# Performance work log

Measured on AMD Instinct MI355X. Metric: run time of the kernel, lower is better.

## Reference

```python
import jax, jax.numpy as jnp
import numpy as np

N = 50000      # nodes
E = 800000     # edges (avg degree 16)
D = 96         # input_size == output_size
C = 10         # n_class
STEPS = 4      # num_layers -> GGNN propagation steps


def setup_inputs() -> dict:
    key = jax.random.key(0)
    ks = jax.random.split(key, 12)
    s = 1.0 / np.sqrt(D)
    return {
        "x": jax.random.normal(ks[0], (N, D), dtype=jnp.float32),
        "src": jax.random.randint(ks[1], (E,), 0, N, dtype=jnp.int32),
        "dst": jax.random.randint(ks[2], (E,), 0, N, dtype=jnp.int32),
        # edge message transform (DGL GatedGraphConv: Linear(out, out) per etype, 1 etype)
        "W_e": jax.random.normal(ks[3], (D, D), dtype=jnp.float32) * s,
        "b_e": jax.random.normal(ks[4], (D,), dtype=jnp.float32) * s,
        # GRUCell params (torch layout: rows ordered r, z, n)
        "W_ih": jax.random.normal(ks[5], (3 * D, D), dtype=jnp.float32) * s,
        "W_hh": jax.random.normal(ks[6], (3 * D, D), dtype=jnp.float32) * s,
        "b_ih": jax.random.normal(ks[7], (3 * D,), dtype=jnp.float32) * s,
        "b_hh": jax.random.normal(ks[8], (3 * D,), dtype=jnp.float32) * s,
        # classifier head
        "W_fc": jax.random.normal(ks[9], (C, D), dtype=jnp.float32) * s,
        "b_fc": jax.random.normal(ks[10], (C,), dtype=jnp.float32) * s,
    }


def _gru_cell(a, h, W_ih, W_hh, b_ih, b_hh):
    # torch.nn.GRUCell math; gate order r, z, n
    gx = a @ W_ih.T + b_ih            # [N, 3D]
    gh = h @ W_hh.T + b_hh            # [N, 3D]
    xr, xz, xn = jnp.split(gx, 3, axis=-1)
    hr, hz, hn = jnp.split(gh, 3, axis=-1)
    r = jax.nn.sigmoid(xr + hr)
    z = jax.nn.sigmoid(xz + hz)
    n = jnp.tanh(xn + r * hn)
    return (1.0 - z) * n + z * h


def reference(x, src, dst, W_e, b_e, W_ih, W_hh, b_ih, b_hh, W_fc, b_fc):
    h = x  # in_feats == out_feats, no padding needed
    for _ in range(STEPS):
        m = h @ W_e.T + b_e                                  # per-node transform [N, D]
        a = jax.ops.segment_sum(m[src], dst, num_segments=N) # gather + scatter-add [N, D]
        h = _gru_cell(a, h, W_ih, W_hh, b_ih, b_hh)
    logits = jax.nn.elu(h) @ W_fc.T + b_fc                   # [N, C]
    return logits
```

## Files before the change

kernel.cpp:

```cpp
#include <hip/hip_runtime.h>

static constexpr int D = 96;
static constexpr int G3 = 3 * D;
static constexpr int NSTEPS = 4;
static constexpr int NT = 18;
static constexpr int SCAN_BLK = 1024;
static constexpr int SLP = 104;

typedef __attribute__((ext_vector_type(8))) _Float16 f16x8;
typedef __attribute__((ext_vector_type(4))) _Float16 f16x4;
typedef __attribute__((ext_vector_type(4))) float f32x4;

__device__ __forceinline__ f16x8 load_a_frag(const _Float16* __restrict__ base,
                                             int r0, int lane, int kc) {
  int row = r0 + (lane & 15);
  int k0 = kc * 32 + ((lane >> 4) << 3);
  return *(const f16x8*)(base + (size_t)row * D + k0);
}

__device__ __forceinline__ f16x8 load_b_swz(const _Float16* __restrict__ W,
                                            int t, int kc, int lane) {
  return *(const f16x8*)(W + (((size_t)t * 3 + kc) * 64 + lane) * 8);
}


__global__ void convert_x_kernel(const float* __restrict__ x,
                                 _Float16* __restrict__ h, int total4) {
  int i = blockIdx.x * blockDim.x + threadIdx.x;
  if (i >= total4) return;
  float4 v = ((const float4*)x)[i];
  f16x4 o;
  o[0] = (_Float16)v.x; o[1] = (_Float16)v.y;
  o[2] = (_Float16)v.z; o[3] = (_Float16)v.w;
  *(f16x4*)(h + (size_t)i * 4) = o;
}

__global__ void compute_wx_kernel(const float* __restrict__ Wih,
                                  const float* __restrict__ We,
                                  const float* __restrict__ be,
                                  float* __restrict__ Wx,
                                  float* __restrict__ bxe) {
  int idx = blockIdx.x * blockDim.x + threadIdx.x;
  if (idx < G3 * D) {
    int r = idx / D, k = idx - r * D;
    float acc = 0.f;
    for (int c = 0; c < D; ++c) acc += Wih[r * D + c] * We[c * D + k];
    Wx[idx] = acc;
  } else if (idx < G3 * D + G3) {
    int r = idx - G3 * D;
    float acc = 0.f;
    for (int c = 0; c < D; ++c) acc += Wih[r * D + c] * be[c];
    bxe[r] = acc;
  }
}

__global__ void swizzle_f16_kernel(const float* __restrict__ Wx,
                                   const float* __restrict__ Whh,
                                   _Float16* __restrict__ WxF,
                                   _Float16* __restrict__ WhhF) {
  int idx = blockIdx.x * blockDim.x + threadIdx.x;
  if (idx >= 2 * NT * 3 * 64) return;
  int mat = idx / (NT * 3 * 64);
  int rem = idx - mat * (NT * 3 * 64);
  int t = rem / (3 * 64);
  int rem2 = rem - t * (3 * 64);
  int kc = rem2 >> 6;
  int lane = rem2 & 63;
  int c = t * 16 + (lane & 15);
  int k0 = kc * 32 + ((lane >> 4) << 3);
  const float* W = mat ? Whh : Wx;
  _Float16* dF = mat ? WhhF : WxF;
  f16x8 o;
#pragma unroll
  for (int j = 0; j < 8; ++j) o[j] = (_Float16)W[(size_t)c * D + k0 + j];
  *(f16x8*)(dF + (((size_t)t * 3 + kc) * 64 + lane) * 8) = o;
}


__global__ void hist_kernel(const int* __restrict__ dst, int* __restrict__ counts, int E) {
  int e = blockIdx.x * blockDim.x + threadIdx.x;
  if (e < E) atomicAdd(&counts[dst[e]], 1);
}

__global__ void partial_sum_kernel(const int* __restrict__ counts,
                                   int* __restrict__ blk_sums, int n) {
  __shared__ int red[256];
  int base = blockIdx.x * SCAN_BLK;
  int tid = threadIdx.x;
  int s = 0;
#pragma unroll
  for (int j = 0; j < 4; ++j) {
    int i = base + j * 256 + tid;
    if (i < n) s += counts[i];
  }
  red[tid] = s;
  __syncthreads();
  for (int off = 128; off > 0; off >>= 1) {
    if (tid < off) red[tid] += red[tid + off];
    __syncthreads();
  }
  if (tid == 0) blk_sums[blockIdx.x] = red[0];
}

__global__ void scan_offsets_kernel(const int* __restrict__ blk_sums,
                                    int* __restrict__ blk_off,
                                    int* __restrict__ row_ptr, int nb, int n) {
  __shared__ int lds[64];
  int tid = threadIdx.x;
  if (tid < nb) lds[tid] = blk_sums[tid];
  __syncthreads();
  if (tid == 0) {
    int run = 0;
    for (int i = 0; i < nb; ++i) { blk_off[i] = run; run += lds[i]; }
    row_ptr[n] = run;
  }
}

__global__ void block_scan_kernel(const int* __restrict__ counts,
                                  const int* __restrict__ blk_off,
                                  int* __restrict__ row_ptr, int n) {
  __shared__ int red[256];
  int base = blockIdx.x * SCAN_BLK;
  int tid = threadIdx.x;
  int i0 = base + tid * 4;
  int v0 = 0, v1 = 0, v2 = 0, v3 = 0;
  if (i0 + 3 < n) {
    int4 c = *(const int4*)(counts + i0);
    v0 = c.x; v1 = c.y; v2 = c.z; v3 = c.w;
  } else {
    if (i0 < n) v0 = counts[i0];
    if (i0 + 1 < n) v1 = counts[i0 + 1];
    if (i0 + 2 < n) v2 = counts[i0 + 2];
  }
  int tsum = v0 + v1 + v2 + v3;
  red[tid] = tsum;
  __syncthreads();
  for (int off = 1; off < 256; off <<= 1) {
    int t = (tid >= off) ? red[tid - off] : 0;
    __syncthreads();
    red[tid] += t;
    __syncthreads();
  }
  int excl = blk_off[blockIdx.x] + red[tid] - tsum;
  if (i0 < n) row_ptr[i0] = excl;
  if (i0 + 1 < n) row_ptr[i0 + 1] = excl + v0;
  if (i0 + 2 < n) row_ptr[i0 + 2] = excl + v0 + v1;
  if (i0 + 3 < n) row_ptr[i0 + 3] = excl + v0 + v1 + v2;
}

__global__ void fill_kernel(const int* __restrict__ src, const int* __restrict__ dst,
                            const int* __restrict__ row_ptr,
                            int* __restrict__ fillc, int* __restrict__ csr_src, int E) {
  int e = blockIdx.x * blockDim.x + threadIdx.x;
  if (e >= E) return;
  int t = dst[e];
  int pos = row_ptr[t] + atomicAdd(&fillc[t], 1);
  csr_src[pos] = src[e];
}


__device__ __forceinline__ void store_planes(float* lds, const f32x4* accM,
                                             const f32x4* accE, int main_plane,
                                             int extra_plane, int extra_ct0, int lane) {
  int col_l = lane & 15;
  int rq = (lane >> 4) << 2;
#pragma unroll
  for (int ct = 0; ct < 6; ++ct)
#pragma unroll
    for (int q = 0; q < 4; ++q)
      lds[main_plane * (16 * D) + (rq + q) * D + ct * 16 + col_l] = accM[ct][q];
#pragma unroll
  for (int ct = 0; ct < 3; ++ct)
#pragma unroll
    for (int q = 0; q < 4; ++q)
      lds[extra_plane * (16 * D) + (rq + q) * D + (extra_ct0 + ct) * 16 + col_l] = accE[ct][q];
}

__device__ __forceinline__ void gru_epilogue(const float* lds,
                                             const _Float16* __restrict__ h,
                                             _Float16* __restrict__ hout,
                                             const int* __restrict__ row_ptr,
                                             const float* __restrict__ bxe,
                                             const float* __restrict__ bih,
                                             const float* __restrict__ bhh,
                                             int base_row, int tid) {
#pragma unroll
  for (int j = 0; j < 6; ++j) {
    int e = tid + j * 256;
    int row = e / D;
    int col = e - row * D;
    int grow = base_row + row;
    float degf = (float)(row_ptr[grow + 1] - row_ptr[grow]);
    float R  = lds[e] + lds[16 * D + e];
    float Z  = lds[2 * 16 * D + e] + lds[3 * 16 * D + e];
    float XN = lds[4 * 16 * D + e];
    float HN = lds[5 * 16 * D + e];
    float rg = 1.0f / (1.0f + __expf(-(R + bih[col] + bhh[col] + degf * bxe[col])));
    float zg = 1.0f / (1.0f + __expf(-(Z + bih[D + col] + bhh[D + col] + degf * bxe[D + col])));
    float ng = tanhf(XN + bih[2 * D + col] + degf * bxe[2 * D + col] + rg * (HN + bhh[2 * D + col]));
    float hv = (float)h[(size_t)grow * D + col];
    hout[(size_t)grow * D + col] = (_Float16)((1.0f - zg) * ng + zg * hv);
  }
}

__global__ __launch_bounds__(256) void gru_fused_kernel(
    const _Float16* __restrict__ h, _Float16* __restrict__ hout,
    const int* __restrict__ row_ptr, const int* __restrict__ csr_src,
    const _Float16* __restrict__ WxF, const _Float16* __restrict__ WhhF,
    const float* __restrict__ bxe, const float* __restrict__ bih,
    const float* __restrict__ bhh, int n) {
  __shared__ float lds[6 * 16 * D];
  __shared__ _Float16 sl[32][SLP];
  int r0 = blockIdx.x << 5;
  int w = threadIdx.x >> 6;
  int lane = threadIdx.x & 63;

  {
    int row = threadIdx.x >> 3;
    int part = threadIdx.x & 7;
    int grow = r0 + row;
    float acc[12];
#pragma unroll
    for (int j = 0; j < 12; ++j) acc[j] = 0.f;
    if (grow < n) {
      int beg = row_ptr[grow], end = row_ptr[grow + 1];
      int e = beg;
      for (; e + 1 < end; e += 2) {
        const _Float16* p0 = h + (size_t)csr_src[e] * D + part * 12;
        const _Float16* p1 = h + (size_t)csr_src[e + 1] * D + part * 12;
        f16x4 u0 = *(const f16x4*)(p0), u1 = *(const f16x4*)(p0 + 4), u2 = *(const f16x4*)(p0 + 8);
        f16x4 v0 = *(const f16x4*)(p1), v1 = *(const f16x4*)(p1 + 4), v2 = *(const f16x4*)(p1 + 8);
#pragma unroll
        for (int j = 0; j < 4; ++j) {
          acc[j]     += (float)u0[j] + (float)v0[j];
          acc[4 + j] += (float)u1[j] + (float)v1[j];
          acc[8 + j] += (float)u2[j] + (float)v2[j];
        }
      }
      if (e < end) {
        const _Float16* p0 = h + (size_t)csr_src[e] * D + part * 12;
        f16x4 u0 = *(const f16x4*)(p0), u1 = *(const f16x4*)(p0 + 4), u2 = *(const f16x4*)(p0 + 8);
#pragma unroll
        for (int j = 0; j < 4; ++j) {
          acc[j] += (float)u0[j]; acc[4 + j] += (float)u1[j]; acc[8 + j] += (float)u2[j];
        }
      }
    }
    f16x4 o0, o1, o2;
#pragma unroll
    for (int j = 0; j < 4; ++j) {
      o0[j] = (_Float16)acc[j]; o1[j] = (_Float16)acc[4 + j]; o2[j] = (_Float16)acc[8 + j];
    }
    *(f16x4*)&sl[row][part * 12]     = o0;
    *(f16x4*)&sl[row][part * 12 + 4] = o1;
    *(f16x4*)&sl[row][part * 12 + 8] = o2;
  }
  __syncthreads();

  const int opS = (w < 2) ? 1 : 0;
  const _Float16* WF = opS ? WxF : WhhF;
  const int half = w & 1;
  const int main_t0 = half * 6;
  const int main_plane = half * 2 + (opS ? 0 : 1);
  const int extra_t0 = 12 + half * 3;
  const int extra_ct0 = half * 3;
  const int extra_plane = opS ? 4 : 5;

  f16x8 a0[3], a1[3];
  if (opS) {
#pragma unroll
    for (int kc = 0; kc < 3; ++kc) {
      int k0 = kc * 32 + ((lane >> 4) << 3);
      a0[kc] = *(const f16x8*)&sl[lane & 15][k0];
      a1[kc] = *(const f16x8*)&sl[16 + (lane & 15)][k0];
    }
  } else {
#pragma unroll
    for (int kc = 0; kc < 3; ++kc) {
      a0[kc] = load_a_frag(h, r0, lane, kc);
      a1[kc] = load_a_frag(h, r0 + 16, lane, kc);
    }
  }

  f32x4 accM0[6], accM1[6], accE0[3], accE1[3];
#pragma unroll
  for (int t = 0; t < 6; ++t) {
    accM0[t] = (f32x4){0.f, 0.f, 0.f, 0.f};
    accM1[t] = (f32x4){0.f, 0.f, 0.f, 0.f};
  }
#pragma unroll
  for (int t = 0; t < 3; ++t) {
    accE0[t] = (f32x4){0.f, 0.f, 0.f, 0.f};
    accE1[t] = (f32x4){0.f, 0.f, 0.f, 0.f};
  }

#pragma unroll
  for (int ct = 0; ct < 6; ++ct)
#pragma unroll
    for (int kc = 0; kc < 3; ++kc) {
      f16x8 b = load_b_swz(WF, main_t0 + ct, kc, lane);
      accM0[ct] = __builtin_amdgcn_mfma_f32_16x16x32_f16(a0[kc], b, accM0[ct], 0, 0, 0);
      accM1[ct] = __builtin_amdgcn_mfma_f32_16x16x32_f16(a1[kc], b, accM1[ct], 0, 0, 0);
    }
#pragma unroll
  for (int ct = 0; ct < 3; ++ct)
#pragma unroll
    for (int kc = 0; kc < 3; ++kc) {
      f16x8 b = load_b_swz(WF, extra_t0 + ct, kc, lane);
      accE0[ct] = __builtin_amdgcn_mfma_f32_16x16x32_f16(a0[kc], b, accE0[ct], 0, 0, 0);
      accE1[ct] = __builtin_amdgcn_mfma_f32_16x16x32_f16(a1[kc], b, accE1[ct], 0, 0, 0);
    }

  __syncthreads();
  store_planes(lds, accM0, accE0, main_plane, extra_plane, extra_ct0, lane);
  __syncthreads();
  gru_epilogue(lds, h, hout, row_ptr, bxe, bih, bhh, r0, threadIdx.x);
  __syncthreads();
  if (r0 + 16 < n) {
    store_planes(lds, accM1, accE1, main_plane, extra_plane, extra_ct0, lane);
    __syncthreads();
    gru_epilogue(lds, h, hout, row_ptr, bxe, bih, bhh, r0 + 16, threadIdx.x);
  }
}

__global__ void head_kernel(const _Float16* __restrict__ h,
                            const float* __restrict__ Wfc,
                            const float* __restrict__ bfc,
                            float* __restrict__ out,
                            int n, int C) {
  int idx = blockIdx.x * blockDim.x + threadIdx.x;
  if (idx >= n * C) return;
  int i = idx / C;
  int c = idx - i * C;
  const _Float16* hr = h + (size_t)i * D;
  const float* wr = Wfc + (size_t)c * D;
  float acc = bfc[c];
#pragma unroll 8
  for (int k = 0; k < D; ++k) {
    float hv = (float)hr[k];
    float e = hv > 0.0f ? hv : (__expf(hv) - 1.0f);
    acc += e * wr[k];
  }
  out[idx] = acc;
}

extern "C" void kernel_launch(void* const* d_in, const int* in_sizes, int n_in,
                              void* d_out, int out_size, void* d_ws, size_t ws_size,
                              hipStream_t stream) {
  const float* x    = (const float*)d_in[0];
  const int*   src  = (const int*)d_in[1];
  const int*   dst  = (const int*)d_in[2];
  const float* W_e  = (const float*)d_in[3];
  const float* b_e  = (const float*)d_in[4];
  const float* W_ih = (const float*)d_in[5];
  const float* W_hh = (const float*)d_in[6];
  const float* b_ih = (const float*)d_in[7];
  const float* b_hh = (const float*)d_in[8];
  const float* W_fc = (const float*)d_in[9];
  const float* b_fc = (const float*)d_in[10];

  const int n = in_sizes[0] / D;
  const int E = in_sizes[1];
  const int C = out_size / n;

  _Float16* hA = (_Float16*)d_ws;
  _Float16* hB = hA + (size_t)n * D;
  float* Wx    = (float*)(hB + (size_t)n * D);
  _Float16* WxF  = (_Float16*)(Wx + (size_t)G3 * D);
  _Float16* WhhF = WxF + (size_t)G3 * D;
  float* bxe   = (float*)(WhhF + (size_t)G3 * D);
  int* counts  = (int*)(bxe + G3);
  int* fillc   = counts + n;
  int* row_ptr = fillc + n;
  int* csr_src = row_ptr + (n + 1);
  int* blk_sums = csr_src + E;
  int* blk_off  = blk_sums + 64;

  const int threads = 256;
  const int nb = (n + SCAN_BLK - 1) / SCAN_BLK;

  (void)hipMemsetAsync(counts, 0, (size_t)2 * n * sizeof(int), stream);
  hist_kernel<<<(E + threads - 1) / threads, threads, 0, stream>>>(dst, counts, E);
  partial_sum_kernel<<<nb, 256, 0, stream>>>(counts, blk_sums, n);
  scan_offsets_kernel<<<1, 64, 0, stream>>>(blk_sums, blk_off, row_ptr, nb, n);
  block_scan_kernel<<<nb, 256, 0, stream>>>(counts, blk_off, row_ptr, n);
  fill_kernel<<<(E + threads - 1) / threads, threads, 0, stream>>>(src, dst, row_ptr,
                                                                   fillc, csr_src, E);
  compute_wx_kernel<<<(G3 * D + G3 + threads - 1) / threads, threads, 0, stream>>>(
      W_ih, W_e, b_e, Wx, bxe);
  swizzle_f16_kernel<<<(2 * NT * 3 * 64 + threads - 1) / threads, threads, 0, stream>>>(
      Wx, W_hh, WxF, WhhF);
  convert_x_kernel<<<((n * D / 4) + threads - 1) / threads, threads, 0, stream>>>(
      x, hA, n * D / 4);

  const int gridG = (n + 31) / 32;

  const _Float16* hcur = hA;
  _Float16* hnext = hB;
  for (int step = 0; step < NSTEPS; ++step) {
    gru_fused_kernel<<<gridG, threads, 0, stream>>>(hcur, hnext, row_ptr, csr_src,
                                                    WxF, WhhF, bxe, b_ih, b_hh, n);
    const _Float16* t = hcur; hcur = hnext; hnext = (_Float16*)t;
  }

  const int gridH = (n * C + threads - 1) / threads;
  head_kernel<<<gridH, threads, 0, stream>>>(hcur, W_fc, b_fc, (float*)d_out, n, C);
}
```

Measured before the change: 362.6 us.

## Use 384-thread blocks with six waves splitting GRU GEMM tiles evenly

The fused GRU kernel moves from 4 to 6 waves per block. Each wave now handles exactly 6 of the 18 output column tiles for one operand, so the separate extra-tile accumulators go away. The gather phase uses 12 threads per row with 16-byte loads and unrolls by four edges, which gives more loads in flight. The LDS planes are padded to a stride of 97 to reduce bank conflicts, and one pre-store barrier is dropped. The larger block and register use per thread may lower occupancy.

New measurement: 356.3 us. Within noise of the previous version (-1.7%).

```diff
diff --git a/kernel.cpp b/kernel.cpp
--- a/kernel.cpp
+++ b/kernel.cpp
@@ -6,6 +6,8 @@
 static constexpr int NT = 18;
 static constexpr int SCAN_BLK = 1024;
 static constexpr int SLP = 104;
+static constexpr int PLS = 97;
+static constexpr int PLANE = 16 * PLS;
 
 typedef __attribute__((ext_vector_type(8))) _Float16 f16x8;
 typedef __attribute__((ext_vector_type(4))) _Float16 f16x4;
@@ -159,23 +161,6 @@
 }
 
 
-__device__ __forceinline__ void store_planes(float* lds, const f32x4* accM,
-                                             const f32x4* accE, int main_plane,
-                                             int extra_plane, int extra_ct0, int lane) {
-  int col_l = lane & 15;
-  int rq = (lane >> 4) << 2;
-#pragma unroll
-  for (int ct = 0; ct < 6; ++ct)
-#pragma unroll
-    for (int q = 0; q < 4; ++q)
-      lds[main_plane * (16 * D) + (rq + q) * D + ct * 16 + col_l] = accM[ct][q];
-#pragma unroll
-  for (int ct = 0; ct < 3; ++ct)
-#pragma unroll
-    for (int q = 0; q < 4; ++q)
-      lds[extra_plane * (16 * D) + (rq + q) * D + (extra_ct0 + ct) * 16 + col_l] = accE[ct][q];
-}
-
 __device__ __forceinline__ void gru_epilogue(const float* lds,
                                              const _Float16* __restrict__ h,
                                              _Float16* __restrict__ hout,
@@ -185,16 +170,17 @@
                                              const float* __restrict__ bhh,
                                              int base_row, int tid) {
 #pragma unroll
-  for (int j = 0; j < 6; ++j) {
-    int e = tid + j * 256;
+  for (int j = 0; j < 4; ++j) {
+    int e = tid + j * 384;
     int row = e / D;
     int col = e - row * D;
     int grow = base_row + row;
+    int a = row * PLS + col;
     float degf = (float)(row_ptr[grow + 1] - row_ptr[grow]);
-    float R  = lds[e] + lds[16 * D + e];
-    float Z  = lds[2 * 16 * D + e] + lds[3 * 16 * D + e];
-    float XN = lds[4 * 16 * D + e];
-    float HN = lds[5 * 16 * D + e];
+    float R  = lds[a] + lds[PLANE + a];
+    float Z  = lds[2 * PLANE + a] + lds[3 * PLANE + a];
+    float XN = lds[4 * PLANE + a];
+    float HN = lds[5 * PLANE + a];
     float rg = 1.0f / (1.0f + __expf(-(R + bih[col] + bhh[col] + degf * bxe[col])));
     float zg = 1.0f / (1.0f + __expf(-(Z + bih[D + col] + bhh[D + col] + degf * bxe[D + col])));
     float ng = tanhf(XN + bih[2 * D + col] + degf * bxe[2 * D + col] + rg * (HN + bhh[2 * D + col]));
@@ -203,68 +189,57 @@
   }
 }
 
-__global__ __launch_bounds__(256) void gru_fused_kernel(
+__global__ __launch_bounds__(384) void gru_fused_kernel(
     const _Float16* __restrict__ h, _Float16* __restrict__ hout,
     const int* __restrict__ row_ptr, const int* __restrict__ csr_src,
     const _Float16* __restrict__ WxF, const _Float16* __restrict__ WhhF,
     const float* __restrict__ bxe, const float* __restrict__ bih,
     const float* __restrict__ bhh, int n) {
-  __shared__ float lds[6 * 16 * D];
+  __shared__ float lds[6 * PLANE];
   __shared__ _Float16 sl[32][SLP];
   int r0 = blockIdx.x << 5;
-  int w = threadIdx.x >> 6;
-  int lane = threadIdx.x & 63;
+  int tid = threadIdx.x;
+  int w = tid >> 6;
+  int lane = tid & 63;
 
   {
-    int row = threadIdx.x >> 3;
-    int part = threadIdx.x & 7;
+    int row = tid / 12;
+    int part = tid - row * 12;
     int grow = r0 + row;
-    float acc[12];
-#pragma unroll
-    for (int j = 0; j < 12; ++j) acc[j] = 0.f;
+    float acc[8];
+#pragma unroll
+    for (int j = 0; j < 8; ++j) acc[j] = 0.f;
     if (grow < n) {
       int beg = row_ptr[grow], end = row_ptr[grow + 1];
       int e = beg;
-      for (; e + 1 < end; e += 2) {
-        const _Float16* p0 = h + (size_t)csr_src[e] * D + part * 12;
-        const _Float16* p1 = h + (size_t)csr_src[e + 1] * D + part * 12;
-        f16x4 u0 = *(const f16x4*)(p0), u1 = *(const f16x4*)(p0 + 4), u2 = *(const f16x4*)(p0 + 8);
-        f16x4 v0 = *(const f16x4*)(p1), v1 = *(const f16x4*)(p1 + 4), v2 = *(const f16x4*)(p1 + 8);
-#pragma unroll
-        for (int j = 0; j < 4; ++j) {
-          acc[j]     += (float)u0[j] + (float)v0[j];
-          acc[4 + j] += (float)u1[j] + (float)v1[j];
-          acc[8 + j] += (float)u2[j] + (float)v2[j];
-        }
+      for (; e + 3 < end; e += 4) {
+        int s0 = csr_src[e], s1 = csr_src[e + 1], s2 = csr_src[e + 2], s3 = csr_src[e + 3];
+        f16x8 v0 = *(const f16x8*)(h + (size_t)s0 * D + part * 8);
+        f16x8 v1 = *(const f16x8*)(h + (size_t)s1 * D + part * 8);
+        f16x8 v2 = *(const f16x8*)(h + (size_t)s2 * D + part * 8);
+        f16x8 v3 = *(const f16x8*)(h + (size_t)s3 * D + part * 8);
+#pragma unroll
+        for (int j = 0; j < 8; ++j)
+          acc[j] += ((float)v0[j] + (float)v1[j]) + ((float)v2[j] + (float)v3[j]);
       }
-      if (e < end) {
-        const _Float16* p0 = h + (size_t)csr_src[e] * D + part * 12;
-        f16x4 u0 = *(const f16x4*)(p0), u1 = *(const f16x4*)(p0 + 4), u2 = *(const f16x4*)(p0 + 8);
-#pragma unroll
-        for (int j = 0; j < 4; ++j) {
-          acc[j] += (float)u0[j]; acc[4 + j] += (float)u1[j]; acc[8 + j] += (float)u2[j];
-        }
+      for (; e < end; ++e) {
+        f16x8 v = *(const f16x8*)(h + (size_t)csr_src[e] * D + part * 8);
+#pragma unroll
+        for (int j = 0; j < 8; ++j) acc[j] += (float)v[j];
       }
     }
-    f16x4 o0, o1, o2;
-#pragma unroll
-    for (int j = 0; j < 4; ++j) {
-      o0[j] = (_Float16)acc[j]; o1[j] = (_Float16)acc[4 + j]; o2[j] = (_Float16)acc[8 + j];
-    }
-    *(f16x4*)&sl[row][part * 12]     = o0;
-    *(f16x4*)&sl[row][part * 12 + 4] = o1;
-    *(f16x4*)&sl[row][part * 12 + 8] = o2;
-  }
-  __syncthreads();
-
-  const int opS = (w < 2) ? 1 : 0;
+    f16x8 o;
+#pragma unroll
+    for (int j = 0; j < 8; ++j) o[j] = (_Float16)acc[j];
+    *(f16x8*)&sl[row][part * 8] = o;
+  }
+  __syncthreads();
+
+  const int opS = (w < 3) ? 1 : 0;
   const _Float16* WF = opS ? WxF : WhhF;
-  const int half = w & 1;
-  const int main_t0 = half * 6;
-  const int main_plane = half * 2 + (opS ? 0 : 1);
-  const int extra_t0 = 12 + half * 3;
-  const int extra_ct0 = half * 3;
-  const int extra_plane = opS ? 4 : 5;
+  const int wg = opS ? w : (w - 3);
+  const int t0 = wg * 6;
+  const int plane = wg * 2 + (opS ? 0 : 1);
 
   f16x8 a0[3], a1[3];
   if (opS) {
@@ -282,44 +257,40 @@
     }
   }
 
-  f32x4 accM0[6], accM1[6], accE0[3], accE1[3];
+  f32x4 acc0[6], acc1[6];
 #pragma unroll
   for (int t = 0; t < 6; ++t) {
-    accM0[t] = (f32x4){0.f, 0.f, 0.f, 0.f};
-    accM1[t] = (f32x4){0.f, 0.f, 0.f, 0.f};
-  }
-#pragma unroll
-  for (int t = 0; t < 3; ++t) {
-    accE0[t] = (f32x4){0.f, 0.f, 0.f, 0.f};
-    accE1[t] = (f32x4){0.f, 0.f, 0.f, 0.f};
+    acc0[t] = (f32x4){0.f, 0.f, 0.f, 0.f};
+    acc1[t] = (f32x4){0.f, 0.f, 0.f, 0.f};
   }
 
 #pragma unroll
   for (int ct = 0; ct < 6; ++ct)
 #pragma unroll
     for (int kc = 0; kc < 3; ++kc) {
-      f16x8 b = load_b_swz(WF, main_t0 + ct, kc, lane);
-      accM0[ct] = __builtin_amdgcn_mfma_f32_16x16x32_f16(a0[kc], b, accM0[ct], 0, 0, 0);
-      accM1[ct] = __builtin_amdgcn_mfma_f32_16x16x32_f16(a1[kc], b, accM1[ct], 0, 0, 0);
+      f16x8 b = load_b_swz(WF, t0 + ct, kc, lane);
+      acc0[ct] = __builtin_amdgcn_mfma_f32_16x16x32_f16(a0[kc], b, acc0[ct], 0, 0, 0);
+      acc1[ct] = __builtin_amdgcn_mfma_f32_16x16x32_f16(a1[kc], b, acc1[ct], 0, 0, 0);
     }
-#pragma unroll
-  for (int ct = 0; ct < 3; ++ct)
-#pragma unroll
-    for (int kc = 0; kc < 3; ++kc) {
-      f16x8 b = load_b_swz(WF, extra_t0 + ct, kc, lane);
-      accE0[ct] = __builtin_amdgcn_mfma_f32_16x16x32_f16(a0[kc], b, accE0[ct], 0, 0, 0);
-      accE1[ct] = __builtin_amdgcn_mfma_f32_16x16x32_f16(a1[kc], b, accE1[ct], 0, 0, 0);
-    }
-
-  __syncthreads();
-  store_planes(lds, accM0, accE0, main_plane, extra_plane, extra_ct0, lane);
-  __syncthreads();
-  gru_epilogue(lds, h, hout, row_ptr, bxe, bih, bhh, r0, threadIdx.x);
+
+  int col_l = lane & 15;
+  int rq = (lane >> 4) << 2;
+#pragma unroll
+  for (int ct = 0; ct < 6; ++ct)
+#pragma unroll
+    for (int q = 0; q < 4; ++q)
+      lds[plane * PLANE + (rq + q) * PLS + ct * 16 + col_l] = acc0[ct][q];
+  __syncthreads();
+  gru_epilogue(lds, h, hout, row_ptr, bxe, bih, bhh, r0, tid);
   __syncthreads();
   if (r0 + 16 < n) {
-    store_planes(lds, accM1, accE1, main_plane, extra_plane, extra_ct0, lane);
+#pragma unroll
+    for (int ct = 0; ct < 6; ++ct)
+#pragma unroll
+      for (int q = 0; q < 4; ++q)
+        lds[plane * PLANE + (rq + q) * PLS + ct * 16 + col_l] = acc1[ct][q];
     __syncthreads();
-    gru_epilogue(lds, h, hout, row_ptr, bxe, bih, bhh, r0 + 16, threadIdx.x);
+    gru_epilogue(lds, h, hout, row_ptr, bxe, bih, bhh, r0 + 16, tid);
   }
 }
 
@@ -398,8 +369,8 @@
   const _Float16* hcur = hA;
   _Float16* hnext = hB;
   for (int step = 0; step < NSTEPS; ++step) {
-    gru_fused_kernel<<<gridG, threads, 0, stream>>>(hcur, hnext, row_ptr, csr_src,
-                                                    WxF, WhhF, bxe, b_ih, b_hh, n);
+    gru_fused_kernel<<<gridG, 384, 0, stream>>>(hcur, hnext, row_ptr, csr_src,
+                                                WxF, WhhF, bxe, b_ih, b_hh, n);
     const _Float16* t = hcur; hcur = hnext; hnext = (_Float16*)t;
   }
 
```
